# Performance work log

Hardware: AMD Instinct MI355X
Metric: run time of the kernel (lower is better)

The kernel has to match this reference:

```python
import jax, jax.numpy as jnp
import numpy as np

N_NODES = 50000
N_EDGES = 1600000
IN_DIM = 128
OUT_DIM = 16
N_HEADS = 8


def setup_inputs() -> dict:
    key = jax.random.key(0)
    ks = jax.random.split(key, 9)
    s = 1.0 / np.sqrt(IN_DIM)
    return {
        "h": jax.random.normal(ks[0], (N_NODES, IN_DIM), jnp.float32),
        "Wq": jax.random.normal(ks[1], (IN_DIM, OUT_DIM * N_HEADS), jnp.float32) * s,
        "bq": jax.random.normal(ks[2], (OUT_DIM * N_HEADS,), jnp.float32) * 0.01,
        "Wk": jax.random.normal(ks[3], (IN_DIM, OUT_DIM * N_HEADS), jnp.float32) * s,
        "bk": jax.random.normal(ks[4], (OUT_DIM * N_HEADS,), jnp.float32) * 0.01,
        "Wv": jax.random.normal(ks[5], (IN_DIM, OUT_DIM * N_HEADS), jnp.float32) * s,
        "bv": jax.random.normal(ks[6], (OUT_DIM * N_HEADS,), jnp.float32) * 0.01,
        "src": jax.random.randint(ks[7], (N_EDGES,), 0, N_NODES, jnp.int32),
        "dst": jax.random.randint(ks[8], (N_EDGES,), 0, N_NODES, jnp.int32),
    }


def reference(h, Wq, bq, Wk, bk, Wv, bv, src, dst):
    n_nodes = h.shape[0]
    # node-wise Q/K/V projections -> [N, H, D]
    Q = (h @ Wq + bq).reshape(n_nodes, N_HEADS, OUT_DIM)
    K = (h @ Wk + bk).reshape(n_nodes, N_HEADS, OUT_DIM)
    V = (h @ Wv + bv).reshape(n_nodes, N_HEADS, OUT_DIM)
    # edge-wise score: (K[src] * Q[dst]).sum(-1), scaled-exp with clamp
    score = jnp.sum(K[src] * Q[dst], axis=-1)  # [E, H]
    score = jnp.exp(jnp.clip(score / np.sqrt(OUT_DIM), -5.0, 5.0))
    # scatter-sum weighted values and normalizers to dst nodes
    msg = V[src] * score[:, :, None]  # [E, H, D]
    wV = jax.ops.segment_sum(msg, dst, num_segments=n_nodes)  # [N, H, D]
    z = jax.ops.segment_sum(score, dst, num_segments=n_nodes)  # [N, H]
    return wV / (z[:, :, None] + 1e-6)
```

## Files before the change

kernel.cpp:

```cpp
#include <hip/hip_runtime.h>
#include <hip/hip_bf16.h>
#include <cstddef>

#define N_NODES 50000
#define N_EDGES 1600000
#define IN_DIM 128
#define OUT_DIM 16
#define N_HEADS 8
#define QKV_DIM 128
#define HS_STRIDE 136
#define OS_STRIDE 392

#define SUBB 3125
#define SUBB_PAD 3136
#define BCAP 1024
#define BH_CHUNK 16384
#define BH_BLOCKS 98

typedef __hip_bfloat16 bf16;
typedef short bf16x8 __attribute__((ext_vector_type(8)));
typedef float f32x4  __attribute__((ext_vector_type(4)));

__device__ __forceinline__ float b2f(bf16 x) { return __bfloat162float(x); }

__device__ __forceinline__ float u16tof(unsigned int u) {
    unsigned int x = u << 16;
    float f;
    __builtin_memcpy(&f, &x, 4);
    return f;
}

__device__ __forceinline__ unsigned short f2bf(float v) {
    bf16 b = __float2bfloat16(v);
    unsigned short u;
    __builtin_memcpy(&u, &b, 2);
    return u;
}

__global__ __launch_bounds__(256) void init_detect_kernel(
    int* __restrict__ p, int nz_words,
    const unsigned short* __restrict__ hraw, int* __restrict__ flag, int nblocks)
{
    __shared__ int red[256];
    int t = threadIdx.x;
    if ((int)blockIdx.x == nblocks - 1) {
        int cnt = 0;
        for (int i = t; i < 8192; i += 256) {
            unsigned short u = hraw[i];
            int e = (u >> 7) & 0xFF;
            if (e == 0xFF || e > 0x85 || (e == 0 && (u & 0x7F) != 0)) cnt++;
        }
        red[t] = cnt;
        __syncthreads();
        for (int s = 128; s > 0; s >>= 1) {
            if (t < s) red[t] += red[t + s];
            __syncthreads();
        }
        if (t == 0) *flag = red[0];
    } else {
        int i = blockIdx.x * 256 + t;
        if (i < nz_words) p[i] = 0;
    }
}

__global__ __launch_bounds__(256) void sentinel_kernel(unsigned short* __restrict__ out, int n) {
    int i = blockIdx.x * 256 + threadIdx.x;
    if (i < n) out[i] = 0x42C8;
}

__global__ __launch_bounds__(256) void prep_kernel(
    const void* __restrict__ Wqr, const void* __restrict__ bqr,
    const void* __restrict__ Wkr, const void* __restrict__ bkr,
    const void* __restrict__ Wvr, const void* __restrict__ bvr,
    const int* __restrict__ flag,
    unsigned short* __restrict__ Wfrag, float* __restrict__ bias_f)
{
    const bool f32 = (*flag > 100);
    int tid = blockIdx.x * 256 + threadIdx.x;

    if (tid < 384) {
        int mat = tid >> 7, c = tid & 127;
        const void* bp = (mat == 0) ? bqr : (mat == 1) ? bkr : bvr;
        bias_f[tid] = f32 ? ((const float*)bp)[c] : b2f(((const bf16*)bp)[c]);
    }
    if (tid >= 6144) return;

    int l  = tid & 63;
    int s  = (tid >> 6) & 3;
    int nt = tid >> 8;
    int n  = nt * 16 + (l & 15);
    int k0 = s * 32 + (l >> 4) * 8;
    int mat = n >> 7, c = n & 127;
    const void* Wp = (mat == 0) ? Wqr : (mat == 1) ? Wkr : Wvr;

    unsigned short v[8];
#pragma unroll
    for (int j = 0; j < 8; ++j) {
        int k = k0 + j;
        float w = f32 ? ((const float*)Wp)[k * QKV_DIM + c]
                      : b2f(((const bf16*)Wp)[k * QKV_DIM + c]);
        v[j] = f2bf(w);
    }
    ushort4* o = (ushort4*)(Wfrag + (size_t)tid * 8);
    o[0] = make_ushort4(v[0], v[1], v[2], v[3]);
    o[1] = make_ushort4(v[4], v[5], v[6], v[7]);
}

__global__ __launch_bounds__(256) void gemm_kernel(
    const void* __restrict__ hraw,
    const unsigned short* __restrict__ Wfrag, const float* __restrict__ bias_f,
    const int* __restrict__ flag,
    unsigned short* __restrict__ Qt, unsigned short* __restrict__ KVt)
{
    __shared__ __align__(16) unsigned short smem[64 * OS_STRIDE];

    const bool f32 = (*flag > 100);
    const int m0  = blockIdx.x * 64;
    const int tid = threadIdx.x;

#pragma unroll
    for (int it = 0; it < 8; ++it) {
        int idx = it * 1024 + tid * 4;
        int r = idx >> 7, k = idx & 127;
        int row = m0 + r;
        ushort4 w4 = make_ushort4(0, 0, 0, 0);
        if (row < N_NODES) {
            if (f32) {
                float4 v4 = ((const float4*)hraw)[(size_t)row * 32 + (k >> 2)];
                w4 = make_ushort4(f2bf(v4.x), f2bf(v4.y), f2bf(v4.z), f2bf(v4.w));
            } else {
                uint2 u = ((const uint2*)hraw)[(size_t)row * 32 + (k >> 2)];
                w4 = make_ushort4((unsigned short)(u.x & 0xffffu), (unsigned short)(u.x >> 16),
                                  (unsigned short)(u.y & 0xffffu), (unsigned short)(u.y >> 16));
            }
        }
        *(ushort4*)&smem[r * HS_STRIDE + k] = w4;
    }
    __syncthreads();

    const int lane = tid & 63;
    const int wave = tid >> 6;
    const int qd   = lane >> 4;
    const int ln15 = lane & 15;

    bf16x8 afr[4][4];
#pragma unroll
    for (int ms = 0; ms < 4; ++ms)
#pragma unroll
        for (int s = 0; s < 4; ++s)
            afr[ms][s] = *(const bf16x8*)&smem[(ms * 16 + ln15) * HS_STRIDE + s * 32 + qd * 8];

    __syncthreads();

#pragma unroll
    for (int i = 0; i < 6; ++i) {
        const int nt  = wave + i * 4;
        const int col = nt * 16 + ln15;
        const float bs = bias_f[col];
        const int mat = col >> 7, c127 = col & 127;
        const int ocol = (mat == 0) ? c127
                       : 128 + 8 * (c127 >> 2) + (c127 & 3) + ((mat == 2) ? 4 : 0);

        bf16x8 bfr[4];
#pragma unroll
        for (int s = 0; s < 4; ++s)
            bfr[s] = *(const bf16x8*)(Wfrag + ((size_t)(nt * 4 + s) * 64 + lane) * 8);

#pragma unroll
        for (int ms = 0; ms < 4; ++ms) {
            f32x4 acc = {0.f, 0.f, 0.f, 0.f};
#pragma unroll
            for (int s = 0; s < 4; ++s)
                acc = __builtin_amdgcn_mfma_f32_16x16x32_bf16(afr[ms][s], bfr[s], acc, 0, 0, 0);
#pragma unroll
            for (int r = 0; r < 4; ++r) {
                int rl = ms * 16 + qd * 4 + r;
                smem[rl * OS_STRIDE + ocol] = f2bf(acc[r] + bs);
            }
        }
    }
    __syncthreads();

    for (int q = tid; q < 1024; q += 256) {
        int row = q >> 4, c = q & 15;
        int grow = m0 + row;
        if (grow < N_NODES)
            ((uint4*)Qt)[grow * 16 + c] = *(const uint4*)&smem[row * OS_STRIDE + c * 8];
    }
    for (int q = tid; q < 2048; q += 256) {
        int row = q >> 5, g = q & 31;
        int grow = m0 + row;
        if (grow < N_NODES)
            ((uint4*)KVt)[grow * 32 + g] = *(const uint4*)&smem[row * OS_STRIDE + 128 + g * 8];
    }
}

__global__ __launch_bounds__(256) void scatter_kernel(const int* __restrict__ src,
                                                      const int* __restrict__ dst,
                                                      int* __restrict__ gcursor,
                                                      unsigned int* __restrict__ packed) {
    __shared__ int lcnt[SUBB];
    __shared__ int lbase[SUBB];
    int t = threadIdx.x;
    for (int i = t; i < SUBB; i += 256) lcnt[i] = 0;
    __syncthreads();
    int base = blockIdx.x * BH_CHUNK;
    for (int i = 0; i < 64; ++i) {
        int e = base + i * 256 + t;
        if (e < N_EDGES) atomicAdd(&lcnt[dst[e] >> 4], 1);
    }
    __syncthreads();
    for (int i = t; i < SUBB; i += 256) {
        int c = lcnt[i];
        lbase[i] = c ? atomicAdd(&gcursor[i], c) : 0;
        lcnt[i] = 0;
    }
    __syncthreads();
    for (int i = 0; i < 64; ++i) {
        int e = base + i * 256 + t;
        if (e < N_EDGES) {
            int d = dst[e];
            int b = d >> 4;
            int pos = lbase[b] + atomicAdd(&lcnt[b], 1);
            if (pos < BCAP)
                packed[b * BCAP + pos] = (unsigned int)src[e] | ((unsigned int)(d & 15) << 16);
        }
    }
}

__global__ __launch_bounds__(256, 8) void bucket_agg_kernel(
    const unsigned short* __restrict__ Qt, const unsigned short* __restrict__ KVt,
    const unsigned int* __restrict__ packed, const int* __restrict__ gcursor,
    const int* __restrict__ flag, void* __restrict__ out)
{
    __shared__ unsigned int   lds_pk[BCAP];
    __shared__ unsigned short lds_src[BCAP];
    __shared__ int cnt16[16], base16[16], cur16[16];

    const int sb = blockIdx.x;
    const int t  = threadIdx.x;
    const int nb = min(gcursor[sb], BCAP);

    if (t < 16) { cnt16[t] = 0; cur16[t] = 0; }
    __syncthreads();

    for (int j = t; j < nb; j += 256) {
        unsigned int pk = packed[sb * BCAP + j];
        lds_pk[j] = pk;
        atomicAdd(&cnt16[(pk >> 16) & 15], 1);
    }
    __syncthreads();
    if (t == 0) {
        int acc = 0;
#pragma unroll
        for (int i = 0; i < 16; ++i) { base16[i] = acc; acc += cnt16[i]; }
    }
    __syncthreads();
    for (int j = t; j < nb; j += 256) {
        unsigned int pk = lds_pk[j];
        int dl = (pk >> 16) & 15;
        int pos = base16[dl] + atomicAdd(&cur16[dl], 1);
        lds_src[pos] = (unsigned short)(pk & 0xffffu);
    }
    __syncthreads();

    const int wave = t >> 6;
    const int lane = t & 63;
    const int half = lane >> 5;
    const int hl   = lane & 31;
    const uint4* KV4 = (const uint4*)KVt;
    const bool of32 = (*flag > 100);

    for (int dl = wave; dl < 16; dl += 4) {
        const int d = sb * 16 + dl;
        uint2 qw = ((const uint2*)Qt)[d * 32 + hl];
        const float q0 = u16tof(qw.x & 0xffffu), q1 = u16tof(qw.x >> 16);
        const float q2 = u16tof(qw.y & 0xffffu), q3 = u16tof(qw.y >> 16);
        const int off = base16[dl];
        const int n   = cnt16[dl];

        float a0 = 0.f, a1 = 0.f, a2 = 0.f, a3 = 0.f, zz = 0.f;

#define CONSUME(KV, SCMASK)                                                     \
        {                                                                       \
            float p = fmaf(u16tof((KV).x & 0xffffu), q0,                        \
                      fmaf(u16tof((KV).x >> 16), q1,                            \
                      fmaf(u16tof((KV).y & 0xffffu), q2,                        \
                           u16tof((KV).y >> 16) * q3)));                        \
            p += __shfl_xor(p, 1);                                              \
            p += __shfl_xor(p, 2);                                              \
            float sc = __expf(__builtin_amdgcn_fmed3f(p * 0.25f, -5.f, 5.f));   \
            sc *= (SCMASK);                                                     \
            a0 = fmaf(u16tof((KV).z & 0xffffu), sc, a0);                        \
            a1 = fmaf(u16tof((KV).z >> 16),     sc, a1);                        \
            a2 = fmaf(u16tof((KV).w & 0xffffu), sc, a2);                        \
            a3 = fmaf(u16tof((KV).w >> 16),     sc, a3);                        \
            zz += sc;                                                           \
        }

        int j = 0;
        for (; j + 16 <= n; j += 16) {
            int e[8];
#pragma unroll
            for (int u = 0; u < 8; ++u) e[u] = lds_src[off + j + 2 * u + half];
            uint4 kv[8];
#pragma unroll
            for (int u = 0; u < 8; ++u) kv[u] = KV4[e[u] * 32 + hl];
#pragma unroll
            for (int u = 0; u < 8; ++u) CONSUME(kv[u], 1.f)
        }
        if (j + 8 <= n) {
            int e[4];
#pragma unroll
            for (int u = 0; u < 4; ++u) e[u] = lds_src[off + j + 2 * u + half];
            uint4 kv[4];
#pragma unroll
            for (int u = 0; u < 4; ++u) kv[u] = KV4[e[u] * 32 + hl];
#pragma unroll
            for (int u = 0; u < 4; ++u) CONSUME(kv[u], 1.f)
            j += 8;
        }
        for (; j + 2 <= n; j += 2) {
            int e = lds_src[off + j + half];
            uint4 kv = KV4[e * 32 + hl];
            CONSUME(kv, 1.f)
        }
        if (j < n) {
            int e = lds_src[off + j];
            uint4 kv = KV4[e * 32 + hl];
            CONSUME(kv, (half == 0) ? 1.f : 0.f)
        }
#undef CONSUME

        a0 += __shfl_xor(a0, 32);
        a1 += __shfl_xor(a1, 32);
        a2 += __shfl_xor(a2, 32);
        a3 += __shfl_xor(a3, 32);
        zz += __shfl_xor(zz, 32);

        const float inv = 1.f / (zz + 1e-6f);
        const float r0 = a0 * inv, r1 = a1 * inv, r2 = a2 * inv, r3 = a3 * inv;

        if (half == 0) {
            if (of32) {
                ((float4*)out)[d * 32 + hl] = make_float4(r0, r1, r2, r3);
            } else {
                unsigned int w0 = ((unsigned int)f2bf(r1) << 16) | f2bf(r0);
                unsigned int w1 = ((unsigned int)f2bf(r3) << 16) | f2bf(r2);
                ((uint2*)out)[d * 32 + hl] = make_uint2(w0, w1);
            }
        }
    }
}

extern "C" void kernel_launch(void* const* d_in, const int* in_sizes, int n_in,
                              void* d_out, int out_size, void* d_ws, size_t ws_size,
                              hipStream_t stream)
{
    const void* h  = d_in[0];
    const void* Wq = d_in[1];
    const void* bq = d_in[2];
    const void* Wk = d_in[3];
    const void* bk = d_in[4];
    const void* Wv = d_in[5];
    const void* bv = d_in[6];
    const int*  src = (const int*)d_in[7];
    const int*  dst = (const int*)d_in[8];

    const size_t NQ = (size_t)N_NODES * QKV_DIM;
    const size_t WFRAG_N = 24 * 4 * 64 * 8;

    const size_t need = 3 * NQ * 2 + WFRAG_N * 2 + 384 * 4
                      + ((size_t)SUBB_PAD + 16) * sizeof(int)
                      + (size_t)SUBB * BCAP * 4;

    if (ws_size < need) {
        sentinel_kernel<<<(out_size + 255) / 256, 256, 0, stream>>>((unsigned short*)d_out, out_size);
        return;
    }

    unsigned short* Qt  = (unsigned short*)d_ws;
    unsigned short* KVt = Qt + NQ;
    unsigned short* Wfrag = KVt + 2 * NQ;
    float* bias_f = (float*)(Wfrag + WFRAG_N);
    int* gcursor = (int*)(bias_f + 384);
    int* flag    = gcursor + SUBB_PAD;
    unsigned int* packed = (unsigned int*)(flag + 16);

    const int nz = SUBB_PAD;
    const int id_blocks = (nz + 255) / 256 + 1;
    init_detect_kernel<<<id_blocks, 256, 0, stream>>>(gcursor, nz,
        (const unsigned short*)h, flag, id_blocks);

    prep_kernel<<<24, 256, 0, stream>>>(Wq, bq, Wk, bk, Wv, bv, flag, Wfrag, bias_f);

    const int gemm_blocks = (N_NODES + 63) / 64;
    gemm_kernel<<<gemm_blocks, 256, 0, stream>>>(h, Wfrag, bias_f, flag, Qt, KVt);

    scatter_kernel<<<BH_BLOCKS, 256, 0, stream>>>(src, dst, gcursor, packed);

    bucket_agg_kernel<<<SUBB, 256, 0, stream>>>(Qt, KVt, packed, gcursor, flag, d_out);
}
```

Before: 298.6 us.

## Fold dtype detection and cursor zeroing into prep kernel; shrink agg unroll

Removes the separate init_detect kernel launch. Each prep block now redundantly runs the input-dtype detection reduction and zeroes the bucket cursors itself, saving one launch and its dependency gap. In the aggregation kernel the 8-wide unrolled gather loop is dropped in favour of a 4-wide loop, and the occupancy hint in launch bounds is removed, trading memory-level parallelism for register pressure. The redundant per-block detection adds a little read traffic in prep, and prep now has no early return for tid >= 6144, which is harmless at 24 blocks.

After: 292.6 us. 2.0% less time.

```diff
diff --git a/kernel.cpp b/kernel.cpp
--- a/kernel.cpp
+++ b/kernel.cpp
@@ -37,53 +37,45 @@
     return u;
 }
 
-__global__ __launch_bounds__(256) void init_detect_kernel(
-    int* __restrict__ p, int nz_words,
-    const unsigned short* __restrict__ hraw, int* __restrict__ flag, int nblocks)
-{
-    __shared__ int red[256];
-    int t = threadIdx.x;
-    if ((int)blockIdx.x == nblocks - 1) {
-        int cnt = 0;
-        for (int i = t; i < 8192; i += 256) {
-            unsigned short u = hraw[i];
-            int e = (u >> 7) & 0xFF;
-            if (e == 0xFF || e > 0x85 || (e == 0 && (u & 0x7F) != 0)) cnt++;
-        }
-        red[t] = cnt;
-        __syncthreads();
-        for (int s = 128; s > 0; s >>= 1) {
-            if (t < s) red[t] += red[t + s];
-            __syncthreads();
-        }
-        if (t == 0) *flag = red[0];
-    } else {
-        int i = blockIdx.x * 256 + t;
-        if (i < nz_words) p[i] = 0;
-    }
-}
-
 __global__ __launch_bounds__(256) void sentinel_kernel(unsigned short* __restrict__ out, int n) {
     int i = blockIdx.x * 256 + threadIdx.x;
     if (i < n) out[i] = 0x42C8;
 }
 
 __global__ __launch_bounds__(256) void prep_kernel(
+    const unsigned short* __restrict__ hraw,
     const void* __restrict__ Wqr, const void* __restrict__ bqr,
     const void* __restrict__ Wkr, const void* __restrict__ bkr,
     const void* __restrict__ Wvr, const void* __restrict__ bvr,
-    const int* __restrict__ flag,
+    int* __restrict__ gcursor, int* __restrict__ flag,
     unsigned short* __restrict__ Wfrag, float* __restrict__ bias_f)
 {
-    const bool f32 = (*flag > 100);
-    int tid = blockIdx.x * 256 + threadIdx.x;
+    __shared__ int red[256];
+    const int t   = threadIdx.x;
+    const int tid = blockIdx.x * 256 + t;
+
+    int cnt = 0;
+    for (int i = t; i < 8192; i += 256) {
+        unsigned short u = hraw[i];
+        int e = (u >> 7) & 0xFF;
+        if (e == 0xFF || e > 0x85 || (e == 0 && (u & 0x7F) != 0)) cnt++;
+    }
+    red[t] = cnt;
+    __syncthreads();
+    for (int s = 128; s > 0; s >>= 1) {
+        if (t < s) red[t] += red[t + s];
+        __syncthreads();
+    }
+    const bool f32 = (red[0] > 100);
+    if (blockIdx.x == 0 && t == 0) *flag = red[0];
+
+    if (tid < SUBB_PAD) gcursor[tid] = 0;
 
     if (tid < 384) {
         int mat = tid >> 7, c = tid & 127;
         const void* bp = (mat == 0) ? bqr : (mat == 1) ? bkr : bvr;
         bias_f[tid] = f32 ? ((const float*)bp)[c] : b2f(((const bf16*)bp)[c]);
     }
-    if (tid >= 6144) return;
 
     int l  = tid & 63;
     int s  = (tid >> 6) & 3;
@@ -228,7 +220,7 @@
     }
 }
 
-__global__ __launch_bounds__(256, 8) void bucket_agg_kernel(
+__global__ __launch_bounds__(256) void bucket_agg_kernel(
     const unsigned short* __restrict__ Qt, const unsigned short* __restrict__ KVt,
     const unsigned int* __restrict__ packed, const int* __restrict__ gcursor,
     const int* __restrict__ flag, void* __restrict__ out)
@@ -299,17 +291,7 @@
         }
 
         int j = 0;
-        for (; j + 16 <= n; j += 16) {
-            int e[8];
-#pragma unroll
-            for (int u = 0; u < 8; ++u) e[u] = lds_src[off + j + 2 * u + half];
-            uint4 kv[8];
-#pragma unroll
-            for (int u = 0; u < 8; ++u) kv[u] = KV4[e[u] * 32 + hl];
-#pragma unroll
-            for (int u = 0; u < 8; ++u) CONSUME(kv[u], 1.f)
-        }
-        if (j + 8 <= n) {
+        for (; j + 8 <= n; j += 8) {
             int e[4];
 #pragma unroll
             for (int u = 0; u < 4; ++u) e[u] = lds_src[off + j + 2 * u + half];
@@ -318,7 +300,6 @@
             for (int u = 0; u < 4; ++u) kv[u] = KV4[e[u] * 32 + hl];
 #pragma unroll
             for (int u = 0; u < 4; ++u) CONSUME(kv[u], 1.f)
-            j += 8;
         }
         for (; j + 2 <= n; j += 2) {
             int e = lds_src[off + j + half];
@@ -387,12 +368,8 @@
     int* flag    = gcursor + SUBB_PAD;
     unsigned int* packed = (unsigned int*)(flag + 16);
 
-    const int nz = SUBB_PAD;
-    const int id_blocks = (nz + 255) / 256 + 1;
-    init_detect_kernel<<<id_blocks, 256, 0, stream>>>(gcursor, nz,
-        (const unsigned short*)h, flag, id_blocks);
-
-    prep_kernel<<<24, 256, 0, stream>>>(Wq, bq, Wk, bk, Wv, bv, flag, Wfrag, bias_f);
+    prep_kernel<<<24, 256, 0, stream>>>((const unsigned short*)h,
+        Wq, bq, Wk, bk, Wv, bv, gcursor, flag, Wfrag, bias_f);
 
     const int gemm_blocks = (N_NODES + 63) / 64;
     gemm_kernel<<<gemm_blocks, 256, 0, stream>>>(h, Wfrag, bias_f, flag, Qt, KVt);
```
